# Kernel optimization log

Hardware: AMD Instinct MI355X
Metric: run time of the kernel (lower is better)

## Reference

```python
import jax, jax.numpy as jnp
import numpy as np

N_EXPERTS = 8
TOP_K = 2


def setup_inputs() -> dict:
    key = jax.random.key(0)
    ks = jax.random.split(key, 5)
    B, S, D = 4, 2048, 1024
    H = 2 * D  # SwiGLU hidden = 2 * embeddings_dims
    E = N_EXPERTS
    scale_d = 1.0 / np.sqrt(D)
    scale_h = 1.0 / np.sqrt(H)
    return {
        "x": jax.random.normal(ks[0], (B, S, D), dtype=jnp.float32),
        "Wg": jax.random.normal(ks[1], (D, E), dtype=jnp.float32) * scale_d,
        "W1": jax.random.normal(ks[2], (E, D, H), dtype=jnp.float32) * scale_d,
        "W2": jax.random.normal(ks[3], (E, D, H), dtype=jnp.float32) * scale_d,
        "W3": jax.random.normal(ks[4], (E, H, D), dtype=jnp.float32) * scale_h,
    }


def _swiglu(x, w1, w2, w3):
    # x: [B,S,D]; w1,w2: [D,H]; w3: [H,D]
    a = x @ w1
    swish = a * jax.nn.sigmoid(a)
    return (swish * (x @ w2)) @ w3


def reference(x, Wg, W1, W2, W3):
    # Gating (noisy_topk disabled -> deterministic path)
    gate = x @ Wg                                   # [B,S,E]
    top_vals, top_idx = jax.lax.top_k(gate, TOP_K)  # [B,S,K]
    probs = jax.nn.softmax(top_vals, axis=-1)       # softmax over top-k values

    out = jnp.zeros_like(x)
    for e in range(N_EXPERTS):
        # combine weight for expert e per token (0 if not routed)
        w_e = jnp.sum(jnp.where(top_idx == e, probs, 0.0), axis=-1)  # [B,S]
        out = out + _swiglu(x, W1[e], W2[e], W3[e]) * w_e[..., None]
    return out
```

## Files before the change

kernel.cpp:

```cpp
#include <hip/hip_runtime.h>
#include <stdint.h>
#include <math.h>

#define NTOK  8192
#define DIM   1024
#define HID   2048
#define NE    8

typedef __attribute__((ext_vector_type(8))) short short8;
typedef __attribute__((ext_vector_type(4))) float f32x4;

__device__ __forceinline__ unsigned short f2bf(float f) {
  union { float f; unsigned u; } a; a.f = f;
  unsigned u = a.u;
  u += 0x7fffu + ((u >> 16) & 1u);
  return (unsigned short)(u >> 16);
}

__device__ __forceinline__ void gl2lds16(const unsigned short* g, unsigned short* l) {
  __builtin_amdgcn_global_load_lds(
      (const __attribute__((address_space(1))) unsigned int*)g,
      (__attribute__((address_space(3))) unsigned int*)l,
      16, 0, 0);
}

__global__ void zero_out_kernel(float4* p, int n4) {
  int i = blockIdx.x * blockDim.x + threadIdx.x;
  if (i < n4) p[i] = make_float4(0.f, 0.f, 0.f, 0.f);
}

__global__ void zero_cnt_kernel(int* cnt) {
  if (threadIdx.x < NE) cnt[threadIdx.x] = 0;
}

__global__ void transpose_cast_kernel(const float* __restrict__ in, unsigned short* __restrict__ out,
                                      int R, int C) {
  __shared__ float tile[32][33];
  int e = blockIdx.z;
  const float* ine = in + (size_t)e * R * C;
  unsigned short* oute = out + (size_t)e * R * C;
  int tx = threadIdx.x, ty = threadIdx.y;
  int c = blockIdx.x * 32 + tx;
  #pragma unroll
  for (int i = 0; i < 32; i += 8) {
    int r = blockIdx.y * 32 + ty + i;
    tile[ty + i][tx] = ine[(size_t)r * C + c];
  }
  __syncthreads();
  int cc = blockIdx.y * 32 + tx;
  #pragma unroll
  for (int i = 0; i < 32; i += 8) {
    int rr = blockIdx.x * 32 + ty + i;
    oute[(size_t)rr * R + cc] = f2bf(tile[tx][ty + i]);
  }
}

__global__ __launch_bounds__(256) void gate_kernel(
    const float* __restrict__ x, const float* __restrict__ Wg,
    unsigned short* __restrict__ xb,
    int* __restrict__ eidx, float* __restrict__ eprob) {
  int wid = threadIdx.x >> 6;
  int lane = threadIdx.x & 63;
  int t = blockIdx.x * 4 + wid;
  const float* xr = x + (size_t)t * DIM;
  unsigned short* xbr = xb + (size_t)t * DIM;
  float acc[NE];
  #pragma unroll
  for (int e = 0; e < NE; e++) acc[e] = 0.f;
  #pragma unroll
  for (int it = 0; it < DIM / 64; it++) {
    int d = it * 64 + lane;
    float xv = xr[d];
    xbr[d] = f2bf(xv);
    const float4* wr = (const float4*)(Wg + d * NE);
    float4 w0 = wr[0], w1 = wr[1];
    acc[0] += xv * w0.x; acc[1] += xv * w0.y; acc[2] += xv * w0.z; acc[3] += xv * w0.w;
    acc[4] += xv * w1.x; acc[5] += xv * w1.y; acc[6] += xv * w1.z; acc[7] += xv * w1.w;
  }
  #pragma unroll
  for (int e = 0; e < NE; e++) {
    float v = acc[e];
    #pragma unroll
    for (int off = 32; off > 0; off >>= 1) v += __shfl_xor(v, off);
    acc[e] = v;
  }
  if (lane == 0) {
    int i0 = 0; float v0 = acc[0];
    #pragma unroll
    for (int e = 1; e < NE; e++) if (acc[e] > v0) { v0 = acc[e]; i0 = e; }
    int i1 = -1; float v1 = -3.4e38f;
    #pragma unroll
    for (int e = 0; e < NE; e++) if (e != i0 && acc[e] > v1) { v1 = acc[e]; i1 = e; }
    float e1 = expf(v1 - v0);
    float p0 = 1.f / (1.f + e1);
    float p1 = e1 / (1.f + e1);
    eidx[t] = i0 | (i1 << 16);
    eprob[2 * t] = p0;
    eprob[2 * t + 1] = p1;
  }
}

__global__ __launch_bounds__(512) void route_kernel(
    const int* __restrict__ eidx, const float* __restrict__ eprob,
    int* __restrict__ cnt, int* __restrict__ tok_list, float* __restrict__ prob_list) {
  __shared__ int lhist[NE];
  __shared__ int gbase[NE];
  int tid = threadIdx.x;
  if (tid < NE) lhist[tid] = 0;
  __syncthreads();
  int t = blockIdx.x * 512 + tid;
  int pk = eidx[t];
  int i0 = pk & 0xffff, i1 = pk >> 16;
  int l0 = atomicAdd(&lhist[i0], 1);
  int l1 = atomicAdd(&lhist[i1], 1);
  __syncthreads();
  if (tid < NE) gbase[tid] = atomicAdd(&cnt[tid], lhist[tid]);
  __syncthreads();
  int s0 = gbase[i0] + l0;
  tok_list[i0 * NTOK + s0] = t;
  prob_list[i0 * NTOK + s0] = eprob[2 * t];
  int s1 = gbase[i1] + l1;
  tok_list[i1 * NTOK + s1] = t;
  prob_list[i1 * NTOK + s1] = eprob[2 * t + 1];
}

__global__ void prefix_kernel(const int* __restrict__ cnt, int* __restrict__ base) {
  if (threadIdx.x == 0) {
    int s = 0;
    for (int e = 0; e < NE; e++) { base[e] = s; s += cnt[e]; }
  }
}

__global__ __launch_bounds__(256, 3) void gemm1_kernel(
    const unsigned short* __restrict__ xb,
    const unsigned short* __restrict__ w1t,
    const unsigned short* __restrict__ w2t,
    const int* __restrict__ cnt, const int* __restrict__ base,
    const int* __restrict__ tok_list,
    unsigned short* __restrict__ hbuf) {
  int e = blockIdx.z;
  int count = cnt[e];
  int mt = blockIdx.y;
  if (mt * 128 >= count) return;
  int nt = blockIdx.x;

  __shared__ __align__(16) unsigned short As[128 * 64];
  __shared__ __align__(16) unsigned short Bs1[64 * 64];
  __shared__ __align__(16) unsigned short Bs2[64 * 64];
  __shared__ int toks[128];

  int tid = threadIdx.x;
  if (tid < 128) {
    int r = mt * 128 + tid;
    toks[tid] = tok_list[e * NTOK + (r < count ? r : 0)];
  }
  __syncthreads();

  int wid = tid >> 6, lane = tid & 63;
  int wm = wid >> 1, wn = wid & 1;
  int m16 = lane & 15, quad = lane >> 4;

  const unsigned short* W1e = w1t + (size_t)e * HID * DIM + (size_t)(nt * 64) * DIM;
  const unsigned short* W2e = w2t + (size_t)e * HID * DIM + (size_t)(nt * 64) * DIM;

  const unsigned short* aptr[4];
  #pragma unroll
  for (int i = 0; i < 4; i++) {
    int slot = wid * 256 + i * 64 + lane;
    int r = slot >> 3, c = slot & 7, g = c ^ (r & 7);
    aptr[i] = xb + (size_t)toks[r] * DIM + g * 8;
  }
  const unsigned short *b1p[2], *b2p[2];
  #pragma unroll
  for (int i = 0; i < 2; i++) {
    int slot = wid * 128 + i * 64 + lane;
    int r = slot >> 3, c = slot & 7, g = c ^ (r & 7);
    b1p[i] = W1e + (size_t)r * DIM + g * 8;
    b2p[i] = W2e + (size_t)r * DIM + g * 8;
  }

  f32x4 acc1[4][2], acc2[4][2];
  f32x4 zz = {0.f, 0.f, 0.f, 0.f};
  #pragma unroll
  for (int i = 0; i < 4; i++)
    #pragma unroll
    for (int j = 0; j < 2; j++) { acc1[i][j] = zz; acc2[i][j] = zz; }

  for (int k0 = 0; k0 < DIM; k0 += 64) {
    #pragma unroll
    for (int i = 0; i < 4; i++)
      gl2lds16(aptr[i] + k0, As + (wid * 256 + i * 64) * 8);
    #pragma unroll
    for (int i = 0; i < 2; i++) {
      gl2lds16(b1p[i] + k0, Bs1 + (wid * 128 + i * 64) * 8);
      gl2lds16(b2p[i] + k0, Bs2 + (wid * 128 + i * 64) * 8);
    }
    __syncthreads();
    #pragma unroll
    for (int ks = 0; ks < 2; ks++) {
      int ga = ks * 4 + quad;
      short8 af[4], b1f[2], b2f[2];
      #pragma unroll
      for (int fm = 0; fm < 4; fm++) {
        int ra = wm * 64 + fm * 16 + m16;
        af[fm] = *(const short8*)(As + ra * 64 + (ga ^ (ra & 7)) * 8);
      }
      #pragma unroll
      for (int fn = 0; fn < 2; fn++) {
        int rb = wn * 32 + fn * 16 + m16;
        b1f[fn] = *(const short8*)(Bs1 + rb * 64 + (ga ^ (rb & 7)) * 8);
        b2f[fn] = *(const short8*)(Bs2 + rb * 64 + (ga ^ (rb & 7)) * 8);
      }
      #pragma unroll
      for (int fm = 0; fm < 4; fm++)
        #pragma unroll
        for (int fn = 0; fn < 2; fn++) {
          acc1[fm][fn] = __builtin_amdgcn_mfma_f32_16x16x32_bf16(af[fm], b1f[fn], acc1[fm][fn], 0, 0, 0);
          acc2[fm][fn] = __builtin_amdgcn_mfma_f32_16x16x32_bf16(af[fm], b2f[fn], acc2[fm][fn], 0, 0, 0);
        }
    }
    __syncthreads();
  }

  int hb = base[e];
  #pragma unroll
  for (int fm = 0; fm < 4; fm++)
    #pragma unroll
    for (int fn = 0; fn < 2; fn++)
      #pragma unroll
      for (int r = 0; r < 4; r++) {
        int row = wm * 64 + fm * 16 + quad * 4 + r;
        if (mt * 128 + row < count) {
          float a = acc1[fm][fn][r];
          float v = acc2[fm][fn][r];
          float h = (a / (1.f + __expf(-a))) * v;
          int col = nt * 64 + wn * 32 + fn * 16 + m16;
          hbuf[(size_t)(hb + mt * 128 + row) * HID + col] = f2bf(h);
        }
      }
}

__global__ __launch_bounds__(256, 3) void gemm2_kernel(
    const unsigned short* __restrict__ hbuf,
    const unsigned short* __restrict__ w3t,
    const int* __restrict__ cnt, const int* __restrict__ base,
    const int* __restrict__ tok_list, const float* __restrict__ prob_list,
    float* __restrict__ out) {
  int e = blockIdx.z;
  int count = cnt[e];
  int mt = blockIdx.y;
  if (mt * 128 >= count) return;
  int nt = blockIdx.x;

  __shared__ __align__(16) unsigned short As[128 * 64];
  __shared__ __align__(16) unsigned short Bs[128 * 64];
  __shared__ int toks[128];
  __shared__ float probs[128];

  int tid = threadIdx.x;
  int hb = base[e];
  if (tid < 128) {
    int r = mt * 128 + tid;
    int rc = (r < count) ? r : 0;
    toks[tid] = tok_list[e * NTOK + rc];
    probs[tid] = prob_list[e * NTOK + rc];
  }
  __syncthreads();

  int wid = tid >> 6, lane = tid & 63;
  int wm = wid >> 1, wn = wid & 1;
  int m16 = lane & 15, quad = lane >> 4;

  const unsigned short* W3e = w3t + (size_t)e * DIM * HID + (size_t)(nt * 128) * HID;

  const unsigned short *aptr[4], *bptr[4];
  #pragma unroll
  for (int i = 0; i < 4; i++) {
    int slot = wid * 256 + i * 64 + lane;
    int r = slot >> 3, c = slot & 7, g = c ^ (r & 7);
    int gr = mt * 128 + r;
    int rc = (gr < count) ? gr : (count - 1);
    aptr[i] = hbuf + (size_t)(hb + rc) * HID + g * 8;
    bptr[i] = W3e + (size_t)r * HID + g * 8;
  }

  f32x4 acc[4][4];
  f32x4 zz = {0.f, 0.f, 0.f, 0.f};
  #pragma unroll
  for (int i = 0; i < 4; i++)
    #pragma unroll
    for (int j = 0; j < 4; j++) acc[i][j] = zz;

  for (int k0 = 0; k0 < HID; k0 += 64) {
    #pragma unroll
    for (int i = 0; i < 4; i++) {
      gl2lds16(aptr[i] + k0, As + (wid * 256 + i * 64) * 8);
      gl2lds16(bptr[i] + k0, Bs + (wid * 256 + i * 64) * 8);
    }
    __syncthreads();
    #pragma unroll
    for (int ks = 0; ks < 2; ks++) {
      int ga = ks * 4 + quad;
      short8 af[4], bf[4];
      #pragma unroll
      for (int fm = 0; fm < 4; fm++) {
        int ra = wm * 64 + fm * 16 + m16;
        af[fm] = *(const short8*)(As + ra * 64 + (ga ^ (ra & 7)) * 8);
      }
      #pragma unroll
      for (int fn = 0; fn < 4; fn++) {
        int rb = wn * 64 + fn * 16 + m16;
        bf[fn] = *(const short8*)(Bs + rb * 64 + (ga ^ (rb & 7)) * 8);
      }
      #pragma unroll
      for (int fm = 0; fm < 4; fm++)
        #pragma unroll
        for (int fn = 0; fn < 4; fn++)
          acc[fm][fn] = __builtin_amdgcn_mfma_f32_16x16x32_bf16(af[fm], bf[fn], acc[fm][fn], 0, 0, 0);
    }
    __syncthreads();
  }

  #pragma unroll
  for (int fm = 0; fm < 4; fm++)
    #pragma unroll
    for (int fn = 0; fn < 4; fn++)
      #pragma unroll
      for (int r = 0; r < 4; r++) {
        int row = wm * 64 + fm * 16 + quad * 4 + r;
        if (mt * 128 + row < count) {
          int tok = toks[row];
          float p = probs[row];
          int col = nt * 128 + wn * 64 + fn * 16 + m16;
          atomicAdd(&out[(size_t)tok * DIM + col], p * acc[fm][fn][r]);
        }
      }
}

extern "C" void kernel_launch(void* const* d_in, const int* in_sizes, int n_in,
                              void* d_out, int out_size, void* d_ws, size_t ws_size,
                              hipStream_t stream) {
  const float* x  = (const float*)d_in[0];
  const float* Wg = (const float*)d_in[1];
  const float* W1 = (const float*)d_in[2];
  const float* W2 = (const float*)d_in[3];
  const float* W3 = (const float*)d_in[4];
  float* out = (float*)d_out;

  char* ws = (char*)d_ws;
  size_t off = 0;
  int* cnt = (int*)(ws + off); off += 256;
  int* base = (int*)(ws + off); off += 256;
  int* eidx = (int*)(ws + off); off += (size_t)NTOK * 4;
  float* eprob = (float*)(ws + off); off += (size_t)NTOK * 2 * 4;
  int* tok_list = (int*)(ws + off); off += (size_t)NE * NTOK * 4;
  float* prob_list = (float*)(ws + off); off += (size_t)NE * NTOK * 4;
  unsigned short* xb  = (unsigned short*)(ws + off); off += (size_t)NTOK * DIM * 2;
  unsigned short* w1t = (unsigned short*)(ws + off); off += (size_t)NE * DIM * HID * 2;
  unsigned short* w2t = (unsigned short*)(ws + off); off += (size_t)NE * DIM * HID * 2;
  unsigned short* w3t = (unsigned short*)(ws + off); off += (size_t)NE * DIM * HID * 2;
  unsigned short* hbuf = (unsigned short*)(ws + off); off += (size_t)NTOK * 2 * HID * 2;

  zero_cnt_kernel<<<1, 64, 0, stream>>>(cnt);
  zero_out_kernel<<<(NTOK * DIM / 4 + 255) / 256, 256, 0, stream>>>((float4*)out, NTOK * DIM / 4);
  gate_kernel<<<NTOK / 4, 256, 0, stream>>>(x, Wg, xb, eidx, eprob);
  transpose_cast_kernel<<<dim3(HID / 32, DIM / 32, NE), dim3(32, 8), 0, stream>>>(W1, w1t, DIM, HID);
  transpose_cast_kernel<<<dim3(HID / 32, DIM / 32, NE), dim3(32, 8), 0, stream>>>(W2, w2t, DIM, HID);
  transpose_cast_kernel<<<dim3(DIM / 32, HID / 32, NE), dim3(32, 8), 0, stream>>>(W3, w3t, HID, DIM);
  route_kernel<<<NTOK / 512, 512, 0, stream>>>(eidx, eprob, cnt, tok_list, prob_list);
  prefix_kernel<<<1, 1, 0, stream>>>(cnt, base);
  gemm1_kernel<<<dim3(HID / 64, NTOK / 128, NE), 256, 0, stream>>>(xb, w1t, w2t, cnt, base, tok_list, hbuf);
  gemm2_kernel<<<dim3(DIM / 128, NTOK / 128, NE), 256, 0, stream>>>(hbuf, w3t, cnt, base, tok_list, prob_list, out);
}
```

Baseline: 554.7 us.

## Replace atomic scatter with expert output buffer and combine kernel; vectorize weight transpose

The second expert GEMM now writes unweighted fp32 results into a per-slot buffer (reusing the w1t workspace) instead of doing atomicAdd into the output, and a new combine kernel gathers each token's two expert rows, weights them by the gate probabilities and writes the output once. This removes the output zeroing pass and atomic contention. The transpose-cast kernel uses 64x64 tiles with float4 loads and 16-byte bf16 stores. The zero-count and prefix kernels are folded into the gate and GEMM kernels. In exchange it adds a 64 MB intermediate write and read plus one extra launch, and relies on w1t being dead once gemm1 has finished.

```diff
diff --git a/kernel.cpp b/kernel.cpp
--- a/kernel.cpp
+++ b/kernel.cpp
@@ -24,41 +24,37 @@
       16, 0, 0);
 }
 
-__global__ void zero_out_kernel(float4* p, int n4) {
-  int i = blockIdx.x * blockDim.x + threadIdx.x;
-  if (i < n4) p[i] = make_float4(0.f, 0.f, 0.f, 0.f);
-}
-
-__global__ void zero_cnt_kernel(int* cnt) {
-  if (threadIdx.x < NE) cnt[threadIdx.x] = 0;
-}
-
-__global__ void transpose_cast_kernel(const float* __restrict__ in, unsigned short* __restrict__ out,
-                                      int R, int C) {
-  __shared__ float tile[32][33];
+__global__ __launch_bounds__(256) void transpose_cast_kernel(
+    const float* __restrict__ in, unsigned short* __restrict__ out, int R, int C) {
+  __shared__ unsigned short tileT[64][72];
   int e = blockIdx.z;
-  const float* ine = in + (size_t)e * R * C;
-  unsigned short* oute = out + (size_t)e * R * C;
-  int tx = threadIdx.x, ty = threadIdx.y;
-  int c = blockIdx.x * 32 + tx;
-  #pragma unroll
-  for (int i = 0; i < 32; i += 8) {
-    int r = blockIdx.y * 32 + ty + i;
-    tile[ty + i][tx] = ine[(size_t)r * C + c];
-  }
-  __syncthreads();
-  int cc = blockIdx.y * 32 + tx;
-  #pragma unroll
-  for (int i = 0; i < 32; i += 8) {
-    int rr = blockIdx.x * 32 + ty + i;
-    oute[(size_t)rr * R + cc] = f2bf(tile[tx][ty + i]);
+  const float* ine = in + (size_t)e * R * C + (size_t)(blockIdx.y * 64) * C + blockIdx.x * 64;
+  unsigned short* oute = out + (size_t)e * R * C + (size_t)(blockIdx.x * 64) * R + blockIdx.y * 64;
+  int t = threadIdx.x;
+  #pragma unroll
+  for (int i = 0; i < 4; i++) {
+    int idx = t + i * 256;
+    int r = idx >> 4, c = (idx & 15) * 4;
+    float4 v = *(const float4*)(ine + (size_t)r * C + c);
+    tileT[c + 0][r] = f2bf(v.x);
+    tileT[c + 1][r] = f2bf(v.y);
+    tileT[c + 2][r] = f2bf(v.z);
+    tileT[c + 3][r] = f2bf(v.w);
+  }
+  __syncthreads();
+  #pragma unroll
+  for (int i = 0; i < 2; i++) {
+    int idx = t + i * 256;
+    int rr = idx >> 3, cc = (idx & 7) * 8;
+    *(uint4*)(oute + (size_t)rr * R + cc) = *(const uint4*)(&tileT[rr][cc]);
   }
 }
 
 __global__ __launch_bounds__(256) void gate_kernel(
     const float* __restrict__ x, const float* __restrict__ Wg,
     unsigned short* __restrict__ xb,
-    int* __restrict__ eidx, float* __restrict__ eprob) {
+    int* __restrict__ eidx, float* __restrict__ eprob, int* __restrict__ cnt) {
+  if (blockIdx.x == 0 && threadIdx.x < NE) cnt[threadIdx.x] = 0;
   int wid = threadIdx.x >> 6;
   int lane = threadIdx.x & 63;
   int t = blockIdx.x * 4 + wid;
@@ -101,8 +97,8 @@
 }
 
 __global__ __launch_bounds__(512) void route_kernel(
-    const int* __restrict__ eidx, const float* __restrict__ eprob,
-    int* __restrict__ cnt, int* __restrict__ tok_list, float* __restrict__ prob_list) {
+    const int* __restrict__ eidx,
+    int* __restrict__ cnt, int* __restrict__ tok_list, int* __restrict__ slotpos) {
   __shared__ int lhist[NE];
   __shared__ int gbase[NE];
   int tid = threadIdx.x;
@@ -117,25 +113,18 @@
   if (tid < NE) gbase[tid] = atomicAdd(&cnt[tid], lhist[tid]);
   __syncthreads();
   int s0 = gbase[i0] + l0;
+  int s1 = gbase[i1] + l1;
   tok_list[i0 * NTOK + s0] = t;
-  prob_list[i0 * NTOK + s0] = eprob[2 * t];
-  int s1 = gbase[i1] + l1;
   tok_list[i1 * NTOK + s1] = t;
-  prob_list[i1 * NTOK + s1] = eprob[2 * t + 1];
-}
-
-__global__ void prefix_kernel(const int* __restrict__ cnt, int* __restrict__ base) {
-  if (threadIdx.x == 0) {
-    int s = 0;
-    for (int e = 0; e < NE; e++) { base[e] = s; s += cnt[e]; }
-  }
+  slotpos[2 * t] = (i0 << 16) | s0;
+  slotpos[2 * t + 1] = (i1 << 16) | s1;
 }
 
 __global__ __launch_bounds__(256, 3) void gemm1_kernel(
     const unsigned short* __restrict__ xb,
     const unsigned short* __restrict__ w1t,
     const unsigned short* __restrict__ w2t,
-    const int* __restrict__ cnt, const int* __restrict__ base,
+    const int* __restrict__ cnt,
     const int* __restrict__ tok_list,
     unsigned short* __restrict__ hbuf) {
   int e = blockIdx.z;
@@ -222,7 +211,9 @@
     __syncthreads();
   }
 
-  int hb = base[e];
+  int hb = 0;
+  #pragma unroll
+  for (int j = 0; j < NE; j++) if (j < e) hb += cnt[j];
   #pragma unroll
   for (int fm = 0; fm < 4; fm++)
     #pragma unroll
@@ -243,30 +234,21 @@
 __global__ __launch_bounds__(256, 3) void gemm2_kernel(
     const unsigned short* __restrict__ hbuf,
     const unsigned short* __restrict__ w3t,
-    const int* __restrict__ cnt, const int* __restrict__ base,
-    const int* __restrict__ tok_list, const float* __restrict__ prob_list,
-    float* __restrict__ out) {
+    const int* __restrict__ cnt,
+    float* __restrict__ ybuf) {
   int e = blockIdx.z;
   int count = cnt[e];
   int mt = blockIdx.y;
   if (mt * 128 >= count) return;
   int nt = blockIdx.x;
+  int hb = 0;
+  #pragma unroll
+  for (int j = 0; j < NE; j++) if (j < e) hb += cnt[j];
 
   __shared__ __align__(16) unsigned short As[128 * 64];
   __shared__ __align__(16) unsigned short Bs[128 * 64];
-  __shared__ int toks[128];
-  __shared__ float probs[128];
 
   int tid = threadIdx.x;
-  int hb = base[e];
-  if (tid < 128) {
-    int r = mt * 128 + tid;
-    int rc = (r < count) ? r : 0;
-    toks[tid] = tok_list[e * NTOK + rc];
-    probs[tid] = prob_list[e * NTOK + rc];
-  }
-  __syncthreads();
-
   int wid = tid >> 6, lane = tid & 63;
   int wm = wid >> 1, wn = wid & 1;
   int m16 = lane & 15, quad = lane >> 4;
@@ -329,12 +311,37 @@
       for (int r = 0; r < 4; r++) {
         int row = wm * 64 + fm * 16 + quad * 4 + r;
         if (mt * 128 + row < count) {
-          int tok = toks[row];
-          float p = probs[row];
           int col = nt * 128 + wn * 64 + fn * 16 + m16;
-          atomicAdd(&out[(size_t)tok * DIM + col], p * acc[fm][fn][r]);
+          ybuf[(size_t)(hb + mt * 128 + row) * DIM + col] = acc[fm][fn][r];
         }
       }
+}
+
+__global__ __launch_bounds__(256) void combine_kernel(
+    const float* __restrict__ ybuf, const int* __restrict__ cnt,
+    const int* __restrict__ slotpos, const float* __restrict__ eprob,
+    float* __restrict__ out) {
+  __shared__ int sbase[NE];
+  if (threadIdx.x == 0) {
+    int s = 0;
+    #pragma unroll
+    for (int e = 0; e < NE; e++) { sbase[e] = s; s += cnt[e]; }
+  }
+  __syncthreads();
+  int t = blockIdx.x;
+  int ps0 = slotpos[2 * t], ps1 = slotpos[2 * t + 1];
+  int r0 = sbase[ps0 >> 16] + (ps0 & 0xffff);
+  int r1 = sbase[ps1 >> 16] + (ps1 & 0xffff);
+  float p0 = eprob[2 * t], p1 = eprob[2 * t + 1];
+  int d = threadIdx.x * 4;
+  float4 y0 = *(const float4*)(ybuf + (size_t)r0 * DIM + d);
+  float4 y1 = *(const float4*)(ybuf + (size_t)r1 * DIM + d);
+  float4 o;
+  o.x = p0 * y0.x + p1 * y1.x;
+  o.y = p0 * y0.y + p1 * y1.y;
+  o.z = p0 * y0.z + p1 * y1.z;
+  o.w = p0 * y0.w + p1 * y1.w;
+  *(float4*)(out + (size_t)t * DIM + d) = o;
 }
 
 extern "C" void kernel_launch(void* const* d_in, const int* in_sizes, int n_in,
@@ -350,25 +357,23 @@
   char* ws = (char*)d_ws;
   size_t off = 0;
   int* cnt = (int*)(ws + off); off += 256;
-  int* base = (int*)(ws + off); off += 256;
   int* eidx = (int*)(ws + off); off += (size_t)NTOK * 4;
   float* eprob = (float*)(ws + off); off += (size_t)NTOK * 2 * 4;
+  int* slotpos = (int*)(ws + off); off += (size_t)NTOK * 2 * 4;
   int* tok_list = (int*)(ws + off); off += (size_t)NE * NTOK * 4;
-  float* prob_list = (float*)(ws + off); off += (size_t)NE * NTOK * 4;
   unsigned short* xb  = (unsigned short*)(ws + off); off += (size_t)NTOK * DIM * 2;
   unsigned short* w1t = (unsigned short*)(ws + off); off += (size_t)NE * DIM * HID * 2;
   unsigned short* w2t = (unsigned short*)(ws + off); off += (size_t)NE * DIM * HID * 2;
   unsigned short* w3t = (unsigned short*)(ws + off); off += (size_t)NE * DIM * HID * 2;
   unsigned short* hbuf = (unsigned short*)(ws + off); off += (size_t)NTOK * 2 * HID * 2;
-
-  zero_cnt_kernel<<<1, 64, 0, stream>>>(cnt);
-  zero_out_kernel<<<(NTOK * DIM / 4 + 255) / 256, 256, 0, stream>>>((float4*)out, NTOK * DIM / 4);
-  gate_kernel<<<NTOK / 4, 256, 0, stream>>>(x, Wg, xb, eidx, eprob);
-  transpose_cast_kernel<<<dim3(HID / 32, DIM / 32, NE), dim3(32, 8), 0, stream>>>(W1, w1t, DIM, HID);
-  transpose_cast_kernel<<<dim3(HID / 32, DIM / 32, NE), dim3(32, 8), 0, stream>>>(W2, w2t, DIM, HID);
-  transpose_cast_kernel<<<dim3(DIM / 32, HID / 32, NE), dim3(32, 8), 0, stream>>>(W3, w3t, HID, DIM);
-  route_kernel<<<NTOK / 512, 512, 0, stream>>>(eidx, eprob, cnt, tok_list, prob_list);
-  prefix_kernel<<<1, 1, 0, stream>>>(cnt, base);
-  gemm1_kernel<<<dim3(HID / 64, NTOK / 128, NE), 256, 0, stream>>>(xb, w1t, w2t, cnt, base, tok_list, hbuf);
-  gemm2_kernel<<<dim3(DIM / 128, NTOK / 128, NE), 256, 0, stream>>>(hbuf, w3t, cnt, base, tok_list, prob_list, out);
-}
+  float* ybuf = (float*)w1t;
+
+  gate_kernel<<<NTOK / 4, 256, 0, stream>>>(x, Wg, xb, eidx, eprob, cnt);
+  transpose_cast_kernel<<<dim3(HID / 64, DIM / 64, NE), 256, 0, stream>>>(W1, w1t, DIM, HID);
+  transpose_cast_kernel<<<dim3(HID / 64, DIM / 64, NE), 256, 0, stream>>>(W2, w2t, DIM, HID);
+  transpose_cast_kernel<<<dim3(DIM / 64, HID / 64, NE), 256, 0, stream>>>(W3, w3t, HID, DIM);
+  route_kernel<<<NTOK / 512, 512, 0, stream>>>(eidx, cnt, tok_list, slotpos);
+  gemm1_kernel<<<dim3(HID / 64, NTOK / 128, NE), 256, 0, stream>>>(xb, w1t, w2t, cnt, tok_list, hbuf);
+  gemm2_kernel<<<dim3(DIM / 128, NTOK / 128, NE), 256, 0, stream>>>(hbuf, w3t, cnt, ybuf);
+  combine_kernel<<<NTOK, 256, 0, stream>>>(ybuf, cnt, slotpos, eprob, out);
+}
```

After: 527.2 us. 5.0% less time.
